# Performance work log

Measured on AMD Instinct MI355X. Metric: run time of the kernel, lower is better.

Reference implementation:

```python
import jax, jax.numpy as jnp
import numpy as np

B, N, F_IN, H, C = 8, 512, 128, 4, 64  # batch, nodes, in-feat, heads, channels
NEG_BIG = -1e10


def setup_inputs() -> dict:
    key = jax.random.key(0)
    ks = jax.random.split(key, 6)
    X = jax.random.normal(ks[0], (B, N, F_IN), dtype=jnp.float32)
    A = (jax.random.uniform(ks[1], (B, N, N)) < 0.05).astype(jnp.float32)
    A = jnp.maximum(A, jnp.eye(N, dtype=jnp.float32)[None])
    kernels = jax.random.normal(ks[2], (H, F_IN, C), dtype=jnp.float32) * 0.1
    biases = jnp.zeros((H, C), dtype=jnp.float32)
    attn_self = jax.random.normal(ks[3], (H, C), dtype=jnp.float32) * 0.1
    attn_neigh = jax.random.normal(ks[4], (H, C), dtype=jnp.float32) * 0.1
    return dict(X=X, A=A, kernels=kernels, biases=biases,
                attn_self=attn_self, attn_neigh=attn_neigh)


def reference(X, A, kernels, biases, attn_self, attn_neigh):
    # per-head linear projection: [B,H,N,C]
    feats = jnp.einsum('bnf,hfc->bhnc', X, kernels)
    # attention logits e_ij = a_self . h_i + a_neigh . h_j
    a_s = jnp.einsum('bhnc,hc->bhn', feats, attn_self)
    a_n = jnp.einsum('bhnc,hc->bhn', feats, attn_neigh)
    coef = a_s[:, :, :, None] + a_n[:, :, None, :]           # [B,H,N,N]
    coef = jnp.where(coef > 0, coef, 0.2 * coef)             # LeakyReLU(0.2)
    coef = coef + NEG_BIG * (1.0 - A[:, None])               # mask non-edges
    attn = jax.nn.softmax(coef, axis=-1)                     # row softmax
    # dropout is identity at inference (Keras test phase)
    out_h = jnp.einsum('bhij,bhjc->bhic', attn, feats) + biases[None, :, None, :]
    # concat heads: [B,N,H*C]
    output = out_h.transpose(0, 2, 1, 3).reshape(B, N, H * C)
    emb = feats.transpose(0, 2, 1, 3).reshape(B, N, H * C)
    # aggregate('maxpooling', output, A): out[b,j,f] = max_i A[b,i,j]*output[b,j,f]
    agg = jnp.max(A[:, :, :, None] * output[:, None, :, :], axis=1)
    out = jnp.concatenate([emb, agg], axis=-1)               # [B,N,2*H*C]
    return jax.nn.relu(out)
```

## Files before the change

kernel.cpp:

```cpp
#include <hip/hip_runtime.h>
#include <stdint.h>
#include <string.h>


#define NN 512
#define NF 128
#define NC 64

typedef __attribute__((ext_vector_type(8))) short short8;
typedef __attribute__((ext_vector_type(4))) float f32x4;

__device__ __forceinline__ uint16_t f2bf(float f) {
    union { float f; uint32_t u; } v; v.f = f;
    uint32_t u = v.u;
    u += 0x7FFF + ((u >> 16) & 1);
    return (uint16_t)(u >> 16);
}

__global__ __launch_bounds__(256) void k1_feats(
    const float* __restrict__ X, const float* __restrict__ Kern,
    const float* __restrict__ a_self, const float* __restrict__ a_neigh,
    float* __restrict__ out, uint16_t* __restrict__ featw,
    float* __restrict__ asw, float* __restrict__ anw)
{
    __shared__ __align__(16) uint16_t Kt[64][136];
    __shared__ float fs[64][65];

    const int tid  = threadIdx.x;
    const int lane = tid & 63;
    const int wave = tid >> 6;
    const int blk  = blockIdx.x;
    const int nt   = blk & 7;
    const int bh   = blk >> 3;
    const int h    = bh & 3;
    const int b    = bh >> 2;
    const int nb   = nt * 64;

    {
        const int f0 = tid >> 1, c0 = (tid & 1) * 32;
        const float* kp = Kern + h * (NF * NC) + f0 * NC + c0;
        #pragma unroll
        for (int s4 = 0; s4 < 8; ++s4) {
            float4 v = *(const float4*)(kp + s4 * 4);
            Kt[c0 + s4 * 4 + 0][f0] = f2bf(v.x);
            Kt[c0 + s4 * 4 + 1][f0] = f2bf(v.y);
            Kt[c0 + s4 * 4 + 2][f0] = f2bf(v.z);
            Kt[c0 + s4 * 4 + 3][f0] = f2bf(v.w);
        }
    }

    const int m = lane & 15;
    const int q = lane >> 4;
    short8 af[4];
    {
        const float* xr = X + ((size_t)(b * NN) + nb + wave * 16 + m) * NF + q * 8;
        #pragma unroll
        for (int kt = 0; kt < 4; ++kt) {
            float4 x0 = *(const float4*)(xr + kt * 32);
            float4 x1 = *(const float4*)(xr + kt * 32 + 4);
            union { uint32_t u[4]; short8 s; } r;
            r.u[0] = (uint32_t)f2bf(x0.x) | ((uint32_t)f2bf(x0.y) << 16);
            r.u[1] = (uint32_t)f2bf(x0.z) | ((uint32_t)f2bf(x0.w) << 16);
            r.u[2] = (uint32_t)f2bf(x1.x) | ((uint32_t)f2bf(x1.y) << 16);
            r.u[3] = (uint32_t)f2bf(x1.z) | ((uint32_t)f2bf(x1.w) << 16);
            af[kt] = r.s;
        }
    }
    __syncthreads();

    #pragma unroll
    for (int ct = 0; ct < 4; ++ct) {
        f32x4 acc = {0.f, 0.f, 0.f, 0.f};
        #pragma unroll
        for (int kt = 0; kt < 4; ++kt) {
            short8 bfr;
            __builtin_memcpy(&bfr, &Kt[ct * 16 + m][kt * 32 + q * 8], 16);
            acc = __builtin_amdgcn_mfma_f32_16x16x32_bf16(af[kt], bfr, acc, 0, 0, 0);
        }
        #pragma unroll
        for (int r = 0; r < 4; ++r)
            fs[wave * 16 + q * 4 + r][ct * 16 + m] = acc[r];
    }

    {
        const float asv = a_self[h * NC + lane];
        const float anv = a_neigh[h * NC + lane];
        for (int rr = 0; rr < 16; ++rr) {
            const int row = wave * 16 + rr;
            float f = fs[row][lane];
            float s1 = f * asv;
            float s2 = f * anv;
            #pragma unroll
            for (int off = 32; off > 0; off >>= 1) {
                s1 += __shfl_xor(s1, off);
                s2 += __shfl_xor(s2, off);
            }
            if (lane == 0) {
                asw[bh * NN + nb + row] = s1;
                anw[bh * NN + nb + row] = s2;
            }
        }
    }
    __syncthreads();

    {
        const int row = tid >> 2, c0 = (tid & 3) * 16;
        float* ow = out + ((size_t)(b * NN) + nb + row) * 512 + h * NC + c0;
        #pragma unroll
        for (int e4 = 0; e4 < 4; ++e4) {
            float4 v;
            v.x = fmaxf(fs[row][c0 + e4 * 4 + 0], 0.f);
            v.y = fmaxf(fs[row][c0 + e4 * 4 + 1], 0.f);
            v.z = fmaxf(fs[row][c0 + e4 * 4 + 2], 0.f);
            v.w = fmaxf(fs[row][c0 + e4 * 4 + 3], 0.f);
            *(float4*)(ow + e4 * 4) = v;
        }
    }

    {
        #pragma unroll
        for (int cc = 0; cc < 16; ++cc) {
            const int c = wave * 16 + cc;
            featw[((size_t)(bh * NC) + c) * NN + nb + lane] = f2bf(fs[lane][c]);
        }
    }
}

__global__ __launch_bounds__(128) void k2_attn(
    const float* __restrict__ A, const uint16_t* __restrict__ featw,
    const float* __restrict__ asw, const float* __restrict__ anw,
    const float* __restrict__ biases, float* __restrict__ out)
{
    __shared__ __align__(16) uint16_t Vt[64][40];
    __shared__ __align__(16) float anl[NN];
    __shared__ float s_lds[2][16];

    const int tid  = threadIdx.x;
    const int lane = tid & 63;
    const int wave = tid >> 6;
    const int blk  = blockIdx.x;
    const int it   = blk & 15;
    const int bh   = blk >> 4;
    const int h    = bh & 3;
    const int b    = bh >> 2;
    const int m    = lane & 15;
    const int q    = lane >> 4;
    const int i    = it * 32 + wave * 16 + m;

    anl[tid]       = anw[bh * NN + tid];
    anl[tid + 128] = anw[bh * NN + tid + 128];
    anl[tid + 256] = anw[bh * NN + tid + 256];
    anl[tid + 384] = anw[bh * NN + tid + 384];

    const float a_si = asw[bh * NN + i];
    const float* Ab  = A + (size_t)b * NN * NN + (size_t)i * NN;

    f32x4 acc[4];
    #pragma unroll
    for (int ct = 0; ct < 4; ++ct) { acc[ct][0]=0.f; acc[ct][1]=0.f; acc[ct][2]=0.f; acc[ct][3]=0.f; }
    float ssum = 0.f;

    float4 a0 = *(const float4*)(Ab + q * 8);
    float4 a1 = *(const float4*)(Ab + q * 8 + 4);

    const int sc = tid >> 1;
    const int sj = (tid & 1) * 16;
    const uint16_t* fwp = featw + ((size_t)(bh * NC) + sc) * NN + sj;

    for (int ch = 0; ch < 16; ++ch) {
        uint4 f0 = *(const uint4*)(fwp + ch * 32);
        uint4 f1 = *(const uint4*)(fwp + ch * 32 + 8);
        *(uint4*)&Vt[sc][sj]     = f0;
        *(uint4*)&Vt[sc][sj + 8] = f1;
        __syncthreads();

        const int nxt = (ch < 15) ? ch + 1 : 15;
        float4 na0 = *(const float4*)(Ab + nxt * 32 + q * 8);
        float4 na1 = *(const float4*)(Ab + nxt * 32 + q * 8 + 4);

        float4 n0 = *(const float4*)&anl[ch * 32 + q * 8];
        float4 n1 = *(const float4*)&anl[ch * 32 + q * 8 + 4];
        float an[8] = {n0.x, n0.y, n0.z, n0.w, n1.x, n1.y, n1.z, n1.w};
        float aj[8] = {a0.x, a0.y, a0.z, a0.w, a1.x, a1.y, a1.z, a1.w};
        float pv[8];
        #pragma unroll
        for (int k = 0; k < 8; ++k) {
            float e = a_si + an[k];
            float l = fmaxf(e, 0.2f * e);
            pv[k] = aj[k] * __expf(l);
            ssum += pv[k];
        }
        union { uint32_t u[4]; short8 s; } afu;
        afu.u[0] = (uint32_t)f2bf(pv[0]) | ((uint32_t)f2bf(pv[1]) << 16);
        afu.u[1] = (uint32_t)f2bf(pv[2]) | ((uint32_t)f2bf(pv[3]) << 16);
        afu.u[2] = (uint32_t)f2bf(pv[4]) | ((uint32_t)f2bf(pv[5]) << 16);
        afu.u[3] = (uint32_t)f2bf(pv[6]) | ((uint32_t)f2bf(pv[7]) << 16);
        short8 afrg = afu.s;

        #pragma unroll
        for (int ct = 0; ct < 4; ++ct) {
            short8 bfr;
            __builtin_memcpy(&bfr, &Vt[ct * 16 + m][q * 8], 16);
            acc[ct] = __builtin_amdgcn_mfma_f32_16x16x32_bf16(afrg, bfr, acc[ct], 0, 0, 0);
        }
        __syncthreads();
        a0 = na0; a1 = na1;
    }

    ssum += __shfl_xor(ssum, 16);
    ssum += __shfl_xor(ssum, 32);
    if (lane < 16) s_lds[wave][lane] = ssum;

    #pragma unroll
    for (int ct = 0; ct < 4; ++ct) {
        const float bias_c = biases[h * NC + ct * 16 + m];
        #pragma unroll
        for (int r = 0; r < 4; ++r) {
            const int row = q * 4 + r;
            const float sinv = 1.f / s_lds[wave][row];
            float o = fmaxf(acc[ct][r] * sinv + bias_c, 0.f);
            const int gi = it * 32 + wave * 16 + row;
            out[((size_t)(b * NN) + gi) * 512 + 256 + h * NC + ct * 16 + m] = o;
        }
    }
}

extern "C" void kernel_launch(void* const* d_in, const int* in_sizes, int n_in,
                              void* d_out, int out_size, void* d_ws, size_t ws_size,
                              hipStream_t stream) {
    (void)in_sizes; (void)n_in; (void)out_size; (void)ws_size;
    const float* X       = (const float*)d_in[0];
    const float* A       = (const float*)d_in[1];
    const float* Kern    = (const float*)d_in[2];
    const float* biases  = (const float*)d_in[3];
    const float* a_self  = (const float*)d_in[4];
    const float* a_neigh = (const float*)d_in[5];
    float* out = (float*)d_out;

    uint16_t* featw = (uint16_t*)d_ws;
    float* asw = (float*)((char*)d_ws + 2097152);
    float* anw = (float*)((char*)d_ws + 2097152 + 65536);

    hipLaunchKernelGGL(k1_feats, dim3(256), dim3(256), 0, stream,
                       X, Kern, a_self, a_neigh, out, featw, asw, anw);
    hipLaunchKernelGGL(k2_attn, dim3(512), dim3(128), 0, stream,
                       A, featw, asw, anw, biases, out);
}
```

Before: 92.71 us.

## Split attention reduction over j across waves and combine partials in LDS

The attention kernel now gives each block 16 query rows and splits the 512 neighbour columns across 4 waves (split-K). Each wave loads its A tiles and bf16 feature fragments straight from global into registers, which removes the per-chunk LDS staging and the two barriers per iteration. Partial accumulators and row sums are then reduced through LDS before normalisation. This doubles the block count and raises memory-level parallelism, at the cost of more registers, an extra LDS reduction, and uncoalesced per-lane 16-byte feature loads.

```diff
diff --git a/kernel.cpp b/kernel.cpp
--- a/kernel.cpp
+++ b/kernel.cpp
@@ -126,62 +126,65 @@
     }
 }
 
-__global__ __launch_bounds__(128) void k2_attn(
+__global__ __launch_bounds__(256) void k2_attn(
     const float* __restrict__ A, const uint16_t* __restrict__ featw,
     const float* __restrict__ asw, const float* __restrict__ anw,
     const float* __restrict__ biases, float* __restrict__ out)
 {
-    __shared__ __align__(16) uint16_t Vt[64][40];
+    __shared__ float accbuf[4][16][65];
+    __shared__ float sbuf[4][16];
     __shared__ __align__(16) float anl[NN];
-    __shared__ float s_lds[2][16];
 
     const int tid  = threadIdx.x;
     const int lane = tid & 63;
     const int wave = tid >> 6;
     const int blk  = blockIdx.x;
-    const int it   = blk & 15;
-    const int bh   = blk >> 4;
+    const int it   = blk & 31;
+    const int bh   = blk >> 5;
     const int h    = bh & 3;
     const int b    = bh >> 2;
     const int m    = lane & 15;
     const int q    = lane >> 4;
-    const int i    = it * 32 + wave * 16 + m;
+    const int i    = it * 16 + m;
 
     anl[tid]       = anw[bh * NN + tid];
-    anl[tid + 128] = anw[bh * NN + tid + 128];
     anl[tid + 256] = anw[bh * NN + tid + 256];
-    anl[tid + 384] = anw[bh * NN + tid + 384];
 
     const float a_si = asw[bh * NN + i];
     const float* Ab  = A + (size_t)b * NN * NN + (size_t)i * NN;
+    const uint16_t* fwb = featw + (size_t)(bh * NC) * NN;
+
+    float4 a0[4], a1[4];
+    #pragma unroll
+    for (int cc = 0; cc < 4; ++cc) {
+        const int ch = wave * 4 + cc;
+        a0[cc] = *(const float4*)(Ab + ch * 32 + q * 8);
+        a1[cc] = *(const float4*)(Ab + ch * 32 + q * 8 + 4);
+    }
+    short8 vf[4][4];
+    #pragma unroll
+    for (int cc = 0; cc < 4; ++cc) {
+        const int ch = wave * 4 + cc;
+        #pragma unroll
+        for (int ct = 0; ct < 4; ++ct)
+            __builtin_memcpy(&vf[cc][ct],
+                             fwb + ((size_t)(ct * 16 + m)) * NN + ch * 32 + q * 8, 16);
+    }
+    __syncthreads();
 
     f32x4 acc[4];
     #pragma unroll
     for (int ct = 0; ct < 4; ++ct) { acc[ct][0]=0.f; acc[ct][1]=0.f; acc[ct][2]=0.f; acc[ct][3]=0.f; }
     float ssum = 0.f;
 
-    float4 a0 = *(const float4*)(Ab + q * 8);
-    float4 a1 = *(const float4*)(Ab + q * 8 + 4);
-
-    const int sc = tid >> 1;
-    const int sj = (tid & 1) * 16;
-    const uint16_t* fwp = featw + ((size_t)(bh * NC) + sc) * NN + sj;
-
-    for (int ch = 0; ch < 16; ++ch) {
-        uint4 f0 = *(const uint4*)(fwp + ch * 32);
-        uint4 f1 = *(const uint4*)(fwp + ch * 32 + 8);
-        *(uint4*)&Vt[sc][sj]     = f0;
-        *(uint4*)&Vt[sc][sj + 8] = f1;
-        __syncthreads();
-
-        const int nxt = (ch < 15) ? ch + 1 : 15;
-        float4 na0 = *(const float4*)(Ab + nxt * 32 + q * 8);
-        float4 na1 = *(const float4*)(Ab + nxt * 32 + q * 8 + 4);
-
+    #pragma unroll
+    for (int cc = 0; cc < 4; ++cc) {
+        const int ch = wave * 4 + cc;
         float4 n0 = *(const float4*)&anl[ch * 32 + q * 8];
         float4 n1 = *(const float4*)&anl[ch * 32 + q * 8 + 4];
         float an[8] = {n0.x, n0.y, n0.z, n0.w, n1.x, n1.y, n1.z, n1.w};
-        float aj[8] = {a0.x, a0.y, a0.z, a0.w, a1.x, a1.y, a1.z, a1.w};
+        float aj[8] = {a0[cc].x, a0[cc].y, a0[cc].z, a0[cc].w,
+                       a1[cc].x, a1[cc].y, a1[cc].z, a1[cc].w};
         float pv[8];
         #pragma unroll
         for (int k = 0; k < 8; ++k) {
@@ -198,30 +201,32 @@
         short8 afrg = afu.s;
 
         #pragma unroll
-        for (int ct = 0; ct < 4; ++ct) {
-            short8 bfr;
-            __builtin_memcpy(&bfr, &Vt[ct * 16 + m][q * 8], 16);
-            acc[ct] = __builtin_amdgcn_mfma_f32_16x16x32_bf16(afrg, bfr, acc[ct], 0, 0, 0);
-        }
-        __syncthreads();
-        a0 = na0; a1 = na1;
+        for (int ct = 0; ct < 4; ++ct)
+            acc[ct] = __builtin_amdgcn_mfma_f32_16x16x32_bf16(afrg, vf[cc][ct], acc[ct], 0, 0, 0);
     }
 
     ssum += __shfl_xor(ssum, 16);
     ssum += __shfl_xor(ssum, 32);
-    if (lane < 16) s_lds[wave][lane] = ssum;
-
-    #pragma unroll
-    for (int ct = 0; ct < 4; ++ct) {
-        const float bias_c = biases[h * NC + ct * 16 + m];
-        #pragma unroll
-        for (int r = 0; r < 4; ++r) {
-            const int row = q * 4 + r;
-            const float sinv = 1.f / s_lds[wave][row];
-            float o = fmaxf(acc[ct][r] * sinv + bias_c, 0.f);
-            const int gi = it * 32 + wave * 16 + row;
-            out[((size_t)(b * NN) + gi) * 512 + 256 + h * NC + ct * 16 + m] = o;
-        }
+    if (lane < 16) sbuf[wave][lane] = ssum;
+
+    #pragma unroll
+    for (int ct = 0; ct < 4; ++ct)
+        #pragma unroll
+        for (int r = 0; r < 4; ++r)
+            accbuf[wave][q * 4 + r][ct * 16 + m] = acc[ct][r];
+    __syncthreads();
+
+    const int col = tid & 63;
+    const int rg  = tid >> 6;
+    const float bias_c = biases[h * NC + col];
+    #pragma unroll
+    for (int rr = 0; rr < 4; ++rr) {
+        const int row = rg * 4 + rr;
+        float s = sbuf[0][row] + sbuf[1][row] + sbuf[2][row] + sbuf[3][row];
+        float v = accbuf[0][row][col] + accbuf[1][row][col] +
+                  accbuf[2][row][col] + accbuf[3][row][col];
+        float o = fmaxf(v / s + bias_c, 0.f);
+        out[((size_t)(b * NN) + it * 16 + row) * 512 + 256 + h * NC + col] = o;
     }
 }
 
@@ -243,6 +248,6 @@
 
     hipLaunchKernelGGL(k1_feats, dim3(256), dim3(256), 0, stream,
                        X, Kern, a_self, a_neigh, out, featw, asw, anw);
-    hipLaunchKernelGGL(k2_attn, dim3(512), dim3(128), 0, stream,
+    hipLaunchKernelGGL(k2_attn, dim3(1024), dim3(256), 0, stream,
                        A, featw, asw, anw, biases, out);
 }
```

Measured after the change: 92.76 us. Within noise of the previous version (+0.1%).
